# Kernel optimization log

Measured on AMD Instinct MI355X. Metric: run time of the kernel, lower is better.

## Reference

```python
import jax, jax.numpy as jnp
import numpy as np

N_NODES = 50000
N_EDGES = 800000
IN_FEATS = 96
HIDDEN = 48


def setup_inputs() -> dict:
    key = jax.random.key(0)
    ks = jax.random.split(key, 16)
    x = jax.random.normal(ks[0], (N_NODES, IN_FEATS), dtype=jnp.float32)
    edge_index = jax.random.randint(ks[1], (2, N_EDGES), 0, N_NODES, dtype=jnp.int32)

    def lin(k, fan_in, fan_out):
        s = 1.0 / np.sqrt(fan_in)
        return jax.random.uniform(k, (fan_in, fan_out), jnp.float32, -s, s)

    return {
        "x": x,
        "edge_index": edge_index,
        # SAGEConv layer 0: in -> hidden
        "w_self0": lin(ks[2], IN_FEATS, HIDDEN),
        "w_neigh0": lin(ks[3], IN_FEATS, HIDDEN),
        "b0": jnp.zeros((HIDDEN,), jnp.float32),
        # SAGEConv layer 1: hidden -> hidden
        "w_self1": lin(ks[4], HIDDEN, HIDDEN),
        "w_neigh1": lin(ks[5], HIDDEN, HIDDEN),
        "b1": jnp.zeros((HIDDEN,), jnp.float32),
        # SAGEConv layer 2: hidden -> hidden
        "w_self2": lin(ks[6], HIDDEN, HIDDEN),
        "w_neigh2": lin(ks[7], HIDDEN, HIDDEN),
        "b2": jnp.zeros((HIDDEN,), jnp.float32),
        # prediction head: hidden -> 1
        "w_pred": lin(ks[8], HIDDEN, 1),
        "b_pred": jnp.zeros((1,), jnp.float32),
    }


def _sage_mean(x, src, dst, deg_inv, w_self, w_neigh, b):
    # mean over in-neighbors: gather src features, segment-sum at dst, / in-degree
    agg = jax.ops.segment_sum(x[src], dst, num_segments=N_NODES) * deg_inv  # [N, F]
    return x @ w_self + agg @ w_neigh + b


def reference(x, edge_index, w_self0, w_neigh0, b0, w_self1, w_neigh1, b1,
              w_self2, w_neigh2, b2, w_pred, b_pred):
    src, dst = edge_index[0], edge_index[1]
    deg = jax.ops.segment_sum(jnp.ones((src.shape[0],), x.dtype), dst,
                              num_segments=N_NODES)
    deg_inv = (1.0 / jnp.maximum(deg, 1.0))[:, None]  # isolated nodes -> 0 agg

    h = jax.nn.relu(_sage_mean(x, src, dst, deg_inv, w_self0, w_neigh0, b0))
    h = jax.nn.relu(_sage_mean(h, src, dst, deg_inv, w_self1, w_neigh1, b1))
    h = jax.nn.relu(_sage_mean(h, src, dst, deg_inv, w_self2, w_neigh2, b2))
    return h @ w_pred + b_pred  # [N, 1]
```

## Files before the change

kernel.cpp:

```cpp
#include <hip/hip_runtime.h>
#include <hip/hip_fp16.h>


constexpr int HID = 48;
constexpr int MAXDEG = 64;
constexpr int GNB = 64;

__device__ __forceinline__ unsigned pack_h2(float a, float b) {
    __half2 h = __floats2half2_rn(a, b);
    return *reinterpret_cast<unsigned*>(&h);
}
__device__ __forceinline__ void acc_u2(float* g, uint2 u) {
    __half2 h0 = *reinterpret_cast<__half2*>(&u.x);
    __half2 h1 = *reinterpret_cast<__half2*>(&u.y);
    float2 f0 = __half22float2(h0), f1 = __half22float2(h1);
    g[0] += f0.x; g[1] += f0.y; g[2] += f1.x; g[3] += f1.y;
}
__device__ __forceinline__ void unpack_u2(float* v, uint2 u) {
    __half2 h0 = *reinterpret_cast<__half2*>(&u.x);
    __half2 h1 = *reinterpret_cast<__half2*>(&u.y);
    float2 f0 = __half22float2(h0), f1 = __half22float2(h1);
    v[0] = f0.x; v[1] = f0.y; v[2] = f1.x; v[3] = f1.y;
}
__device__ __forceinline__ void fma12_h(const uint2* __restrict__ wrow, float s,
                                        float* acc) {
    uint2 w0 = wrow[0], w1 = wrow[1], w2 = wrow[2];
    float v[12];
    unpack_u2(v + 0, w0); unpack_u2(v + 4, w1); unpack_u2(v + 8, w2);
#pragma unroll
    for (int j = 0; j < 12; ++j) acc[j] = fmaf(s, v[j], acc[j]);
}

__device__ __forceinline__ void gather_h8(const __half* __restrict__ p,
                                          const unsigned short* __restrict__ bkt,
                                          uint4 pv0, uint4 pv1, int deg, int e,
                                          int jb, int zrow, float* g) {
    float ga[12], gb[12];
#pragma unroll
    for (int j = 0; j < 12; ++j) { ga[j] = 0.0f; gb[j] = 0.0f; }
    const int sh = 16 * e;
    int idx[8];
    {
        unsigned w[8] = {pv0.x, pv0.y, pv0.z, pv0.w, pv1.x, pv1.y, pv1.z, pv1.w};
#pragma unroll
        for (int r = 0; r < 8; ++r) {
            int k = 2 * r + e;
            idx[r] = (k < deg) ? (int)((w[r] >> sh) & 0xffffu) : zrow;
        }
    }
    {
        const uint2* r0 = reinterpret_cast<const uint2*>(p + (size_t)idx[0] * HID + jb);
        const uint2* r1 = reinterpret_cast<const uint2*>(p + (size_t)idx[1] * HID + jb);
        const uint2* r2 = reinterpret_cast<const uint2*>(p + (size_t)idx[2] * HID + jb);
        const uint2* r3 = reinterpret_cast<const uint2*>(p + (size_t)idx[3] * HID + jb);
        uint2 a0 = r0[0], a1 = r0[1], a2 = r0[2];
        uint2 b0 = r1[0], b1 = r1[1], b2 = r1[2];
        uint2 c0 = r2[0], c1 = r2[1], c2 = r2[2];
        uint2 d0 = r3[0], d1 = r3[1], d2 = r3[2];
        acc_u2(ga + 0, a0); acc_u2(ga + 4, a1); acc_u2(ga + 8, a2);
        acc_u2(gb + 0, b0); acc_u2(gb + 4, b1); acc_u2(gb + 8, b2);
        acc_u2(ga + 0, c0); acc_u2(ga + 4, c1); acc_u2(ga + 8, c2);
        acc_u2(gb + 0, d0); acc_u2(gb + 4, d1); acc_u2(gb + 8, d2);
    }
    {
        const uint2* r0 = reinterpret_cast<const uint2*>(p + (size_t)idx[4] * HID + jb);
        const uint2* r1 = reinterpret_cast<const uint2*>(p + (size_t)idx[5] * HID + jb);
        const uint2* r2 = reinterpret_cast<const uint2*>(p + (size_t)idx[6] * HID + jb);
        const uint2* r3 = reinterpret_cast<const uint2*>(p + (size_t)idx[7] * HID + jb);
        uint2 a0 = r0[0], a1 = r0[1], a2 = r0[2];
        uint2 b0 = r1[0], b1 = r1[1], b2 = r1[2];
        uint2 c0 = r2[0], c1 = r2[1], c2 = r2[2];
        uint2 d0 = r3[0], d1 = r3[1], d2 = r3[2];
        acc_u2(ga + 0, a0); acc_u2(ga + 4, a1); acc_u2(ga + 8, a2);
        acc_u2(gb + 0, b0); acc_u2(gb + 4, b1); acc_u2(gb + 8, b2);
        acc_u2(ga + 0, c0); acc_u2(ga + 4, c1); acc_u2(ga + 8, c2);
        acc_u2(gb + 0, d0); acc_u2(gb + 4, d1); acc_u2(gb + 8, d2);
    }
    int i = 16 + e;
    for (; i + 6 < deg; i += 8) {
        int s0 = bkt[i], s1 = bkt[i + 2], s2 = bkt[i + 4], s3 = bkt[i + 6];
        const uint2* r0 = reinterpret_cast<const uint2*>(p + (size_t)s0 * HID + jb);
        const uint2* r1 = reinterpret_cast<const uint2*>(p + (size_t)s1 * HID + jb);
        const uint2* r2 = reinterpret_cast<const uint2*>(p + (size_t)s2 * HID + jb);
        const uint2* r3 = reinterpret_cast<const uint2*>(p + (size_t)s3 * HID + jb);
        uint2 a0 = r0[0], a1 = r0[1], a2 = r0[2];
        uint2 b0 = r1[0], b1 = r1[1], b2 = r1[2];
        uint2 c0 = r2[0], c1 = r2[1], c2 = r2[2];
        uint2 d0 = r3[0], d1 = r3[1], d2 = r3[2];
        acc_u2(ga + 0, a0); acc_u2(ga + 4, a1); acc_u2(ga + 8, a2);
        acc_u2(gb + 0, b0); acc_u2(gb + 4, b1); acc_u2(gb + 8, b2);
        acc_u2(ga + 0, c0); acc_u2(ga + 4, c1); acc_u2(ga + 8, c2);
        acc_u2(gb + 0, d0); acc_u2(gb + 4, d1); acc_u2(gb + 8, d2);
    }
    for (; i + 2 < deg; i += 4) {
        int s0 = bkt[i], s1 = bkt[i + 2];
        const uint2* r0 = reinterpret_cast<const uint2*>(p + (size_t)s0 * HID + jb);
        const uint2* r1 = reinterpret_cast<const uint2*>(p + (size_t)s1 * HID + jb);
        uint2 a0 = r0[0], a1 = r0[1], a2 = r0[2];
        uint2 b0 = r1[0], b1 = r1[1], b2 = r1[2];
        acc_u2(ga + 0, a0); acc_u2(ga + 4, a1); acc_u2(ga + 8, a2);
        acc_u2(gb + 0, b0); acc_u2(gb + 4, b1); acc_u2(gb + 8, b2);
    }
    if (i < deg) {
        const uint2* r0 = reinterpret_cast<const uint2*>(p + (size_t)bkt[i] * HID + jb);
        uint2 a0 = r0[0], a1 = r0[1], a2 = r0[2];
        acc_u2(ga + 0, a0); acc_u2(ga + 4, a1); acc_u2(ga + 8, a2);
    }
#pragma unroll
    for (int j = 0; j < 12; ++j) g[j] = ga[j] + gb[j];
#pragma unroll
    for (int j = 0; j < 12; ++j) g[j] += __shfl_xor(g[j], 4, 64);
}

__global__ __launch_bounds__(128) void fill_proj_k(
    const float* __restrict__ X, const float* __restrict__ Wn,
    const float* __restrict__ Ws, const float* __restrict__ bias,
    __half* __restrict__ p_out, float* __restrict__ s_out, int n_nodes,
    const int* __restrict__ src, const int* __restrict__ dst,
    int* __restrict__ cnt, unsigned short* __restrict__ buckets,
    int n_edges, int gemm_blocks, int cstride) {
    __shared__ float wlds[96 * HID];
    __shared__ float bias_lds[HID];
    const int t = threadIdx.x;

    if ((int)blockIdx.x >= gemm_blocks) {
        int base = (blockIdx.x - gemm_blocks) * 512 + t;
#pragma unroll
        for (int u = 0; u < 4; ++u) {
            int eidx = base + u * 128;
            if (eidx < n_edges) {
                int d = dst[eidx];
                int s = src[eidx];
                int pos = atomicAdd(&cnt[(size_t)d * cstride], 1);
                if (pos < MAXDEG) buckets[(size_t)d * MAXDEG + pos] = (unsigned short)s;
            }
        }
        return;
    }

    if (blockIdx.x == 0 && t < 24)
        reinterpret_cast<unsigned*>(p_out + (size_t)n_nodes * HID)[t] = 0u;

    const int q = t & 3;
    const int m = t >> 2;
    const int jb = q * 12;
    const int n0 = blockIdx.x * GNB + 2 * m;
    const int n1 = n0 + 1;
    const bool v0 = n0 < n_nodes, v1 = n1 < n_nodes;
    const int cn0 = v0 ? n0 : 0, cn1 = v1 ? n1 : 0;
    const float4* xr0 = reinterpret_cast<const float4*>(X + (size_t)cn0 * 96);
    const float4* xr1 = reinterpret_cast<const float4*>(X + (size_t)cn1 * 96);

    for (int i = t; i < 96 * HID; i += 128) wlds[i] = Wn[i];
    __syncthreads();
    {
        float pa[12], pb[12];
#pragma unroll
        for (int j = 0; j < 12; ++j) { pa[j] = 0.0f; pb[j] = 0.0f; }
#pragma unroll 4
        for (int k4 = 0; k4 < 24; ++k4) {
            float4 xa = xr0[k4];
            float4 xb = xr1[k4];
#pragma unroll
            for (int c = 0; c < 4; ++c) {
                float x0 = (c == 0) ? xa.x : (c == 1) ? xa.y : (c == 2) ? xa.z : xa.w;
                float x1 = (c == 0) ? xb.x : (c == 1) ? xb.y : (c == 2) ? xb.z : xb.w;
                const float4* wr =
                    reinterpret_cast<const float4*>(&wlds[(k4 * 4 + c) * HID + jb]);
#pragma unroll
                for (int j4 = 0; j4 < 3; ++j4) {
                    float4 wv = wr[j4];
                    pa[j4 * 4 + 0] = fmaf(x0, wv.x, pa[j4 * 4 + 0]);
                    pa[j4 * 4 + 1] = fmaf(x0, wv.y, pa[j4 * 4 + 1]);
                    pa[j4 * 4 + 2] = fmaf(x0, wv.z, pa[j4 * 4 + 2]);
                    pa[j4 * 4 + 3] = fmaf(x0, wv.w, pa[j4 * 4 + 3]);
                    pb[j4 * 4 + 0] = fmaf(x1, wv.x, pb[j4 * 4 + 0]);
                    pb[j4 * 4 + 1] = fmaf(x1, wv.y, pb[j4 * 4 + 1]);
                    pb[j4 * 4 + 2] = fmaf(x1, wv.z, pb[j4 * 4 + 2]);
                    pb[j4 * 4 + 3] = fmaf(x1, wv.w, pb[j4 * 4 + 3]);
                }
            }
        }
        if (v0) {
            uint2* po = reinterpret_cast<uint2*>(p_out + (size_t)n0 * HID + jb);
            po[0] = make_uint2(pack_h2(pa[0], pa[1]), pack_h2(pa[2], pa[3]));
            po[1] = make_uint2(pack_h2(pa[4], pa[5]), pack_h2(pa[6], pa[7]));
            po[2] = make_uint2(pack_h2(pa[8], pa[9]), pack_h2(pa[10], pa[11]));
        }
        if (v1) {
            uint2* po = reinterpret_cast<uint2*>(p_out + (size_t)n1 * HID + jb);
            po[0] = make_uint2(pack_h2(pb[0], pb[1]), pack_h2(pb[2], pb[3]));
            po[1] = make_uint2(pack_h2(pb[4], pb[5]), pack_h2(pb[6], pb[7]));
            po[2] = make_uint2(pack_h2(pb[8], pb[9]), pack_h2(pb[10], pb[11]));
        }
    }
    __syncthreads();

    for (int i = t; i < 96 * HID; i += 128) wlds[i] = Ws[i];
    if (t < HID) bias_lds[t] = bias[t];
    __syncthreads();
    {
        float sa[12], sb[12];
#pragma unroll
        for (int j = 0; j < 12; ++j) {
            float b = bias_lds[jb + j];
            sa[j] = b; sb[j] = b;
        }
#pragma unroll 4
        for (int k4 = 0; k4 < 24; ++k4) {
            float4 xa = xr0[k4];
            float4 xb = xr1[k4];
#pragma unroll
            for (int c = 0; c < 4; ++c) {
                float x0 = (c == 0) ? xa.x : (c == 1) ? xa.y : (c == 2) ? xa.z : xa.w;
                float x1 = (c == 0) ? xb.x : (c == 1) ? xb.y : (c == 2) ? xb.z : xb.w;
                const float4* wr =
                    reinterpret_cast<const float4*>(&wlds[(k4 * 4 + c) * HID + jb]);
#pragma unroll
                for (int j4 = 0; j4 < 3; ++j4) {
                    float4 wv = wr[j4];
                    sa[j4 * 4 + 0] = fmaf(x0, wv.x, sa[j4 * 4 + 0]);
                    sa[j4 * 4 + 1] = fmaf(x0, wv.y, sa[j4 * 4 + 1]);
                    sa[j4 * 4 + 2] = fmaf(x0, wv.z, sa[j4 * 4 + 2]);
                    sa[j4 * 4 + 3] = fmaf(x0, wv.w, sa[j4 * 4 + 3]);
                    sb[j4 * 4 + 0] = fmaf(x1, wv.x, sb[j4 * 4 + 0]);
                    sb[j4 * 4 + 1] = fmaf(x1, wv.y, sb[j4 * 4 + 1]);
                    sb[j4 * 4 + 2] = fmaf(x1, wv.z, sb[j4 * 4 + 2]);
                    sb[j4 * 4 + 3] = fmaf(x1, wv.w, sb[j4 * 4 + 3]);
                }
            }
        }
        float4* so0 = reinterpret_cast<float4*>(s_out + (size_t)cn0 * HID + jb);
        float4* so1 = reinterpret_cast<float4*>(s_out + (size_t)cn1 * HID + jb);
#pragma unroll
        for (int j4 = 0; j4 < 3; ++j4) {
            if (v0) so0[j4] = make_float4(sa[j4 * 4 + 0], sa[j4 * 4 + 1],
                                          sa[j4 * 4 + 2], sa[j4 * 4 + 3]);
            if (v1) so1[j4] = make_float4(sb[j4 * 4 + 0], sb[j4 * 4 + 1],
                                          sb[j4 * 4 + 2], sb[j4 * 4 + 3]);
        }
    }
}

__global__ __launch_bounds__(128, 6) void act_k(
    const __half* __restrict__ p_in, const float* __restrict__ s_in,
    const int* __restrict__ cnt, const unsigned short* __restrict__ buckets,
    __half* __restrict__ h_out, int n_nodes, int cstride) {
    const int t = threadIdx.x;
    if (blockIdx.x == 0 && t < 24)
        reinterpret_cast<unsigned*>(h_out + (size_t)n_nodes * HID)[t] = 0u;
    const int q = t & 3;
    const int e = (t >> 2) & 1;
    const int m = t >> 3;
    const int n = blockIdx.x * 16 + m;
    if (n >= n_nodes) return;
    const int jb = q * 12;

    const int deg_raw = cnt[(size_t)n * cstride];
    const unsigned short* bkt = buckets + (size_t)n * MAXDEG;
    const uint4 pv0 = reinterpret_cast<const uint4*>(bkt)[0];
    const uint4 pv1 = reinterpret_cast<const uint4*>(bkt)[1];
    float4 sv0, sv1, sv2;
    if (e == 0) {
        const float4* sr = reinterpret_cast<const float4*>(s_in + (size_t)n * HID + jb);
        sv0 = sr[0]; sv1 = sr[1]; sv2 = sr[2];
    }

    const int deg = min(deg_raw, MAXDEG);
    const float di = 1.0f / fmaxf((float)deg, 1.0f);
    float g[12];
    gather_h8(p_in, bkt, pv0, pv1, deg, e, jb, n_nodes, g);

    if (e == 0) {
        float h[12];
        h[0] = fmaxf(fmaf(di, g[0], sv0.x), 0.0f);
        h[1] = fmaxf(fmaf(di, g[1], sv0.y), 0.0f);
        h[2] = fmaxf(fmaf(di, g[2], sv0.z), 0.0f);
        h[3] = fmaxf(fmaf(di, g[3], sv0.w), 0.0f);
        h[4] = fmaxf(fmaf(di, g[4], sv1.x), 0.0f);
        h[5] = fmaxf(fmaf(di, g[5], sv1.y), 0.0f);
        h[6] = fmaxf(fmaf(di, g[6], sv1.z), 0.0f);
        h[7] = fmaxf(fmaf(di, g[7], sv1.w), 0.0f);
        h[8] = fmaxf(fmaf(di, g[8], sv2.x), 0.0f);
        h[9] = fmaxf(fmaf(di, g[9], sv2.y), 0.0f);
        h[10] = fmaxf(fmaf(di, g[10], sv2.z), 0.0f);
        h[11] = fmaxf(fmaf(di, g[11], sv2.w), 0.0f);
        uint2* ho = reinterpret_cast<uint2*>(h_out + (size_t)n * HID + jb);
        ho[0] = make_uint2(pack_h2(h[0], h[1]), pack_h2(h[2], h[3]));
        ho[1] = make_uint2(pack_h2(h[4], h[5]), pack_h2(h[6], h[7]));
        ho[2] = make_uint2(pack_h2(h[8], h[9]), pack_h2(h[10], h[11]));
    }
}

template <bool LAST>
__global__ __launch_bounds__(128, 6) void layer_k(
    const __half* __restrict__ h_in, const int* __restrict__ cnt,
    const unsigned short* __restrict__ buckets, const float* __restrict__ wn,
    const float* __restrict__ ws, const float* __restrict__ bn,
    const float* __restrict__ w_pred, const float* __restrict__ b_pred,
    __half* __restrict__ h_out, float* __restrict__ out, int n_nodes,
    int cstride) {
    __shared__ uint2 wn_s[HID * HID / 4];
    __shared__ uint2 ws_s[HID * HID / 4];
    __shared__ float bn_lds[HID];
    __shared__ float wp_lds[HID];

    const int t = threadIdx.x;
    const int q = t & 3;
    const int e = (t >> 2) & 1;
    const int m = t >> 3;
    const int n = blockIdx.x * 16 + m;
    const bool nv = n < n_nodes;
    const int cn = nv ? n : 0;
    const int jb = q * 12;

    if (!LAST && blockIdx.x == 0 && t < 24)
        reinterpret_cast<unsigned*>(h_out + (size_t)n_nodes * HID)[t] = 0u;

    const int deg_raw = cnt[(size_t)cn * cstride];
    const unsigned short* bkt = buckets + (size_t)cn * MAXDEG;
    const uint4 pv0 = reinterpret_cast<const uint4*>(bkt)[0];
    const uint4 pv1 = reinterpret_cast<const uint4*>(bkt)[1];
    const uint2* hr = reinterpret_cast<const uint2*>(h_in + (size_t)cn * HID + jb);
    uint2 ha = hr[0], hb = hr[1], hc = hr[2];

    for (int i4 = t; i4 < HID * HID / 4; i4 += 128) {
        float4 a = reinterpret_cast<const float4*>(wn)[i4];
        float4 b = reinterpret_cast<const float4*>(ws)[i4];
        wn_s[i4] = make_uint2(pack_h2(a.x, a.y), pack_h2(a.z, a.w));
        ws_s[i4] = make_uint2(pack_h2(b.x, b.y), pack_h2(b.z, b.w));
    }
    if (t < HID) bn_lds[t] = bn[t];
    if (LAST && t < HID) wp_lds[t] = w_pred[t];
    __syncthreads();

    if (!nv) return;

    const int deg = min(deg_raw, MAXDEG);
    const float di = 1.0f / fmaxf((float)deg, 1.0f);
    float g[12];
    gather_h8(h_in, bkt, pv0, pv1, deg, e, jb, n_nodes, g);
#pragma unroll
    for (int j = 0; j < 12; ++j) g[j] *= di;

    float hs_own[12];
    unpack_u2(hs_own + 0, ha); unpack_u2(hs_own + 4, hb); unpack_u2(hs_own + 8, hc);

    float acc[12];
#pragma unroll
    for (int j = 0; j < 12; ++j) acc[j] = (e == 0) ? bn_lds[jb + j] : 0.0f;

    const int kb = e * 24;
#pragma unroll
    for (int kk = 0; kk < 24; ++kk) {
        const int k = kb + kk;
        const int srcl = (t & ~3) | (k / 12);
        float gs = __shfl(g[kk % 12], srcl, 64);
        float hv = __shfl(hs_own[kk % 12], srcl, 64);
        fma12_h(&wn_s[(k * HID + jb) >> 2], gs, acc);
        fma12_h(&ws_s[(k * HID + jb) >> 2], hv, acc);
    }
#pragma unroll
    for (int j = 0; j < 12; ++j) acc[j] += __shfl_xor(acc[j], 4, 64);

    if (LAST) {
        float s = 0.0f;
#pragma unroll
        for (int j = 0; j < 12; ++j) s = fmaf(fmaxf(acc[j], 0.0f), wp_lds[jb + j], s);
        s += __shfl_xor(s, 1, 64);
        s += __shfl_xor(s, 2, 64);
        if ((t & 7) == 0) out[n] = s + b_pred[0];
        return;
    }

    if (e == 0) {
        float h[12];
#pragma unroll
        for (int j = 0; j < 12; ++j) h[j] = fmaxf(acc[j], 0.0f);
        uint2* ho = reinterpret_cast<uint2*>(h_out + (size_t)n * HID + jb);
        ho[0] = make_uint2(pack_h2(h[0], h[1]), pack_h2(h[2], h[3]));
        ho[1] = make_uint2(pack_h2(h[4], h[5]), pack_h2(h[6], h[7]));
        ho[2] = make_uint2(pack_h2(h[8], h[9]), pack_h2(h[10], h[11]));
    }
}

extern "C" void kernel_launch(void* const* d_in, const int* in_sizes, int n_in,
                              void* d_out, int out_size, void* d_ws, size_t ws_size,
                              hipStream_t stream) {
    const float* x        = (const float*)d_in[0];
    const int*   ei       = (const int*)d_in[1];
    const float* w_self0  = (const float*)d_in[2];
    const float* w_neigh0 = (const float*)d_in[3];
    const float* b0       = (const float*)d_in[4];
    const float* w_self1  = (const float*)d_in[5];
    const float* w_neigh1 = (const float*)d_in[6];
    const float* b1       = (const float*)d_in[7];
    const float* w_self2  = (const float*)d_in[8];
    const float* w_neigh2 = (const float*)d_in[9];
    const float* b2       = (const float*)d_in[10];
    const float* w_pred   = (const float*)d_in[11];
    const float* b_pred   = (const float*)d_in[12];

    const int n_nodes = in_sizes[0] / 96;
    const int n_edges = in_sizes[1] / 2;
    const int* src = ei;
    const int* dst = ei + n_edges;

    const size_t need_fixed = (size_t)n_nodes * MAXDEG * 2
                            + 3 * ((size_t)(n_nodes + 1) * HID * 2)
                            + (size_t)n_nodes * HID * 4;
    int cstride = (need_fixed + (size_t)n_nodes * 4 * 4 <= ws_size) ? 4 : 1;

    char* wsb = (char*)d_ws;
    int* cnt                = (int*)wsb;              wsb += (size_t)n_nodes * cstride * 4;
    unsigned short* buckets = (unsigned short*)wsb;   wsb += (size_t)n_nodes * MAXDEG * 2;
    __half* p0 = (__half*)wsb;                        wsb += (size_t)(n_nodes + 1) * HID * 2;
    __half* h1 = (__half*)wsb;                        wsb += (size_t)(n_nodes + 1) * HID * 2;
    __half* h2 = (__half*)wsb;                        wsb += (size_t)(n_nodes + 1) * HID * 2;
    float* s0 = (float*)wsb;                          wsb += (size_t)n_nodes * HID * 4;
    float* out = (float*)d_out;

    const int gnb = (n_nodes + GNB - 1) / GNB;
    const int fb = (n_edges + 511) / 512;
    const int lb = (n_nodes + 15) / 16;

    hipMemsetAsync(cnt, 0, (size_t)n_nodes * cstride * 4, stream);

    fill_proj_k<<<gnb + fb, 128, 0, stream>>>(x, w_neigh0, w_self0, b0, p0, s0,
                                              n_nodes, src, dst, cnt, buckets,
                                              n_edges, gnb, cstride);
    act_k<<<lb, 128, 0, stream>>>(p0, s0, cnt, buckets, h1, n_nodes, cstride);
    layer_k<false><<<lb, 128, 0, stream>>>(h1, cnt, buckets, w_neigh1, w_self1,
                                           b1, nullptr, nullptr, h2, nullptr,
                                           n_nodes, cstride);
    layer_k<true><<<lb, 128, 0, stream>>>(h2, cnt, buckets, w_neigh2, w_self2,
                                          b2, w_pred, b_pred, nullptr, out,
                                          n_nodes, cstride);
}
```

Measured before the change: 216.6 us.

## Gather neighbor rows with 16-byte loads, six lanes per node

Changes the gather lane mapping. Before, 8 lanes per node split the edges between two halves and each lane read 12 fp16 channels as three 8-byte loads. Now 6 of the 8 lanes each own 8 channels, read them with one 16-byte load per neighbor over all edges, and need no cross-lane reduction. The aim is fewer, wider memory instructions and no shuffle reduction. In exchange, 2 of every 8 lanes sit idle during the gather, each active lane walks twice as many edges, and the layer kernel's shuffle indexing is rewritten to match the new channel ownership.

Measured after the change: 280.3 us. 1.29x slower.

```diff
diff --git a/kernel.cpp b/kernel.cpp
--- a/kernel.cpp
+++ b/kernel.cpp
@@ -16,6 +16,10 @@
     float2 f0 = __half22float2(h0), f1 = __half22float2(h1);
     g[0] += f0.x; g[1] += f0.y; g[2] += f1.x; g[3] += f1.y;
 }
+__device__ __forceinline__ void acc_u4(float* g, uint4 u) {
+    acc_u2(g + 0, make_uint2(u.x, u.y));
+    acc_u2(g + 4, make_uint2(u.z, u.w));
+}
 __device__ __forceinline__ void unpack_u2(float* v, uint2 u) {
     __half2 h0 = *reinterpret_cast<__half2*>(&u.x);
     __half2 h1 = *reinterpret_cast<__half2*>(&u.y);
@@ -31,85 +35,51 @@
     for (int j = 0; j < 12; ++j) acc[j] = fmaf(s, v[j], acc[j]);
 }
 
-__device__ __forceinline__ void gather_h8(const __half* __restrict__ p,
-                                          const unsigned short* __restrict__ bkt,
-                                          uint4 pv0, uint4 pv1, int deg, int e,
-                                          int jb, int zrow, float* g) {
-    float ga[12], gb[12];
-#pragma unroll
-    for (int j = 0; j < 12; ++j) { ga[j] = 0.0f; gb[j] = 0.0f; }
-    const int sh = 16 * e;
-    int idx[8];
-    {
-        unsigned w[8] = {pv0.x, pv0.y, pv0.z, pv0.w, pv1.x, pv1.y, pv1.z, pv1.w};
-#pragma unroll
-        for (int r = 0; r < 8; ++r) {
-            int k = 2 * r + e;
-            idx[r] = (k < deg) ? (int)((w[r] >> sh) & 0xffffu) : zrow;
-        }
-    }
-    {
-        const uint2* r0 = reinterpret_cast<const uint2*>(p + (size_t)idx[0] * HID + jb);
-        const uint2* r1 = reinterpret_cast<const uint2*>(p + (size_t)idx[1] * HID + jb);
-        const uint2* r2 = reinterpret_cast<const uint2*>(p + (size_t)idx[2] * HID + jb);
-        const uint2* r3 = reinterpret_cast<const uint2*>(p + (size_t)idx[3] * HID + jb);
-        uint2 a0 = r0[0], a1 = r0[1], a2 = r0[2];
-        uint2 b0 = r1[0], b1 = r1[1], b2 = r1[2];
-        uint2 c0 = r2[0], c1 = r2[1], c2 = r2[2];
-        uint2 d0 = r3[0], d1 = r3[1], d2 = r3[2];
-        acc_u2(ga + 0, a0); acc_u2(ga + 4, a1); acc_u2(ga + 8, a2);
-        acc_u2(gb + 0, b0); acc_u2(gb + 4, b1); acc_u2(gb + 8, b2);
-        acc_u2(ga + 0, c0); acc_u2(ga + 4, c1); acc_u2(ga + 8, c2);
-        acc_u2(gb + 0, d0); acc_u2(gb + 4, d1); acc_u2(gb + 8, d2);
-    }
-    {
-        const uint2* r0 = reinterpret_cast<const uint2*>(p + (size_t)idx[4] * HID + jb);
-        const uint2* r1 = reinterpret_cast<const uint2*>(p + (size_t)idx[5] * HID + jb);
-        const uint2* r2 = reinterpret_cast<const uint2*>(p + (size_t)idx[6] * HID + jb);
-        const uint2* r3 = reinterpret_cast<const uint2*>(p + (size_t)idx[7] * HID + jb);
-        uint2 a0 = r0[0], a1 = r0[1], a2 = r0[2];
-        uint2 b0 = r1[0], b1 = r1[1], b2 = r1[2];
-        uint2 c0 = r2[0], c1 = r2[1], c2 = r2[2];
-        uint2 d0 = r3[0], d1 = r3[1], d2 = r3[2];
-        acc_u2(ga + 0, a0); acc_u2(ga + 4, a1); acc_u2(ga + 8, a2);
-        acc_u2(gb + 0, b0); acc_u2(gb + 4, b1); acc_u2(gb + 8, b2);
-        acc_u2(ga + 0, c0); acc_u2(ga + 4, c1); acc_u2(ga + 8, c2);
-        acc_u2(gb + 0, d0); acc_u2(gb + 4, d1); acc_u2(gb + 8, d2);
-    }
-    int i = 16 + e;
-    for (; i + 6 < deg; i += 8) {
-        int s0 = bkt[i], s1 = bkt[i + 2], s2 = bkt[i + 4], s3 = bkt[i + 6];
-        const uint2* r0 = reinterpret_cast<const uint2*>(p + (size_t)s0 * HID + jb);
-        const uint2* r1 = reinterpret_cast<const uint2*>(p + (size_t)s1 * HID + jb);
-        const uint2* r2 = reinterpret_cast<const uint2*>(p + (size_t)s2 * HID + jb);
-        const uint2* r3 = reinterpret_cast<const uint2*>(p + (size_t)s3 * HID + jb);
-        uint2 a0 = r0[0], a1 = r0[1], a2 = r0[2];
-        uint2 b0 = r1[0], b1 = r1[1], b2 = r1[2];
-        uint2 c0 = r2[0], c1 = r2[1], c2 = r2[2];
-        uint2 d0 = r3[0], d1 = r3[1], d2 = r3[2];
-        acc_u2(ga + 0, a0); acc_u2(ga + 4, a1); acc_u2(ga + 8, a2);
-        acc_u2(gb + 0, b0); acc_u2(gb + 4, b1); acc_u2(gb + 8, b2);
-        acc_u2(ga + 0, c0); acc_u2(ga + 4, c1); acc_u2(ga + 8, c2);
-        acc_u2(gb + 0, d0); acc_u2(gb + 4, d1); acc_u2(gb + 8, d2);
-    }
-    for (; i + 2 < deg; i += 4) {
-        int s0 = bkt[i], s1 = bkt[i + 2];
-        const uint2* r0 = reinterpret_cast<const uint2*>(p + (size_t)s0 * HID + jb);
-        const uint2* r1 = reinterpret_cast<const uint2*>(p + (size_t)s1 * HID + jb);
-        uint2 a0 = r0[0], a1 = r0[1], a2 = r0[2];
-        uint2 b0 = r1[0], b1 = r1[1], b2 = r1[2];
-        acc_u2(ga + 0, a0); acc_u2(ga + 4, a1); acc_u2(ga + 8, a2);
-        acc_u2(gb + 0, b0); acc_u2(gb + 4, b1); acc_u2(gb + 8, b2);
-    }
-    if (i < deg) {
-        const uint2* r0 = reinterpret_cast<const uint2*>(p + (size_t)bkt[i] * HID + jb);
-        uint2 a0 = r0[0], a1 = r0[1], a2 = r0[2];
-        acc_u2(ga + 0, a0); acc_u2(ga + 4, a1); acc_u2(ga + 8, a2);
-    }
-#pragma unroll
-    for (int j = 0; j < 12; ++j) g[j] = ga[j] + gb[j];
-#pragma unroll
-    for (int j = 0; j < 12; ++j) g[j] += __shfl_xor(g[j], 4, 64);
+__device__ __forceinline__ void gather8(const __half* __restrict__ p,
+                                        const unsigned short* __restrict__ bkt,
+                                        const uint4 (&pw)[2], int deg,
+                                        int coff, int zrow, float* g) {
+    float ga[8], gb[8];
+#pragma unroll
+    for (int c = 0; c < 8; ++c) { ga[c] = 0.0f; gb[c] = 0.0f; }
+#pragma unroll
+    for (int b = 0; b < 2; ++b) {
+        const int k0 = 8 * b;
+        const unsigned w0 = pw[b].x, w1 = pw[b].y, w2 = pw[b].z, w3 = pw[b].w;
+        int i0 = (k0 + 0 < deg) ? (int)(w0 & 0xffffu) : zrow;
+        int i1 = (k0 + 1 < deg) ? (int)(w0 >> 16) : zrow;
+        int i2 = (k0 + 2 < deg) ? (int)(w1 & 0xffffu) : zrow;
+        int i3 = (k0 + 3 < deg) ? (int)(w1 >> 16) : zrow;
+        int i4 = (k0 + 4 < deg) ? (int)(w2 & 0xffffu) : zrow;
+        int i5 = (k0 + 5 < deg) ? (int)(w2 >> 16) : zrow;
+        int i6 = (k0 + 6 < deg) ? (int)(w3 & 0xffffu) : zrow;
+        int i7 = (k0 + 7 < deg) ? (int)(w3 >> 16) : zrow;
+        uint4 a0 = *reinterpret_cast<const uint4*>(p + (size_t)i0 * HID + coff);
+        uint4 a1 = *reinterpret_cast<const uint4*>(p + (size_t)i1 * HID + coff);
+        uint4 a2 = *reinterpret_cast<const uint4*>(p + (size_t)i2 * HID + coff);
+        uint4 a3 = *reinterpret_cast<const uint4*>(p + (size_t)i3 * HID + coff);
+        uint4 a4 = *reinterpret_cast<const uint4*>(p + (size_t)i4 * HID + coff);
+        uint4 a5 = *reinterpret_cast<const uint4*>(p + (size_t)i5 * HID + coff);
+        uint4 a6 = *reinterpret_cast<const uint4*>(p + (size_t)i6 * HID + coff);
+        uint4 a7 = *reinterpret_cast<const uint4*>(p + (size_t)i7 * HID + coff);
+        acc_u4(ga, a0); acc_u4(gb, a1); acc_u4(ga, a2); acc_u4(gb, a3);
+        acc_u4(ga, a4); acc_u4(gb, a5); acc_u4(ga, a6); acc_u4(gb, a7);
+    }
+    int i = 16;
+    for (; i + 3 < deg; i += 4) {
+        int s0 = bkt[i], s1 = bkt[i + 1], s2 = bkt[i + 2], s3 = bkt[i + 3];
+        uint4 a0 = *reinterpret_cast<const uint4*>(p + (size_t)s0 * HID + coff);
+        uint4 a1 = *reinterpret_cast<const uint4*>(p + (size_t)s1 * HID + coff);
+        uint4 a2 = *reinterpret_cast<const uint4*>(p + (size_t)s2 * HID + coff);
+        uint4 a3 = *reinterpret_cast<const uint4*>(p + (size_t)s3 * HID + coff);
+        acc_u4(ga, a0); acc_u4(gb, a1); acc_u4(ga, a2); acc_u4(gb, a3);
+    }
+    for (; i < deg; ++i) {
+        uint4 a0 = *reinterpret_cast<const uint4*>(p + (size_t)bkt[i] * HID + coff);
+        acc_u4(ga, a0);
+    }
+#pragma unroll
+    for (int c = 0; c < 8; ++c) g[c] = ga[c] + gb[c];
 }
 
 __global__ __launch_bounds__(128) void fill_proj_k(
@@ -249,47 +219,42 @@
     const int t = threadIdx.x;
     if (blockIdx.x == 0 && t < 24)
         reinterpret_cast<unsigned*>(h_out + (size_t)n_nodes * HID)[t] = 0u;
-    const int q = t & 3;
-    const int e = (t >> 2) & 1;
+
+    const int cid = t & 7;
     const int m = t >> 3;
     const int n = blockIdx.x * 16 + m;
     if (n >= n_nodes) return;
-    const int jb = q * 12;
+    const bool active = cid < 6;
+    const int cb = active ? 8 * cid : 0;
 
     const int deg_raw = cnt[(size_t)n * cstride];
     const unsigned short* bkt = buckets + (size_t)n * MAXDEG;
-    const uint4 pv0 = reinterpret_cast<const uint4*>(bkt)[0];
-    const uint4 pv1 = reinterpret_cast<const uint4*>(bkt)[1];
-    float4 sv0, sv1, sv2;
-    if (e == 0) {
-        const float4* sr = reinterpret_cast<const float4*>(s_in + (size_t)n * HID + jb);
-        sv0 = sr[0]; sv1 = sr[1]; sv2 = sr[2];
-    }
+    uint4 pw[2];
+#pragma unroll
+    for (int b = 0; b < 2; ++b) pw[b] = reinterpret_cast<const uint4*>(bkt)[b];
+
+    if (!active) return;
 
     const int deg = min(deg_raw, MAXDEG);
     const float di = 1.0f / fmaxf((float)deg, 1.0f);
-    float g[12];
-    gather_h8(p_in, bkt, pv0, pv1, deg, e, jb, n_nodes, g);
-
-    if (e == 0) {
-        float h[12];
-        h[0] = fmaxf(fmaf(di, g[0], sv0.x), 0.0f);
-        h[1] = fmaxf(fmaf(di, g[1], sv0.y), 0.0f);
-        h[2] = fmaxf(fmaf(di, g[2], sv0.z), 0.0f);
-        h[3] = fmaxf(fmaf(di, g[3], sv0.w), 0.0f);
-        h[4] = fmaxf(fmaf(di, g[4], sv1.x), 0.0f);
-        h[5] = fmaxf(fmaf(di, g[5], sv1.y), 0.0f);
-        h[6] = fmaxf(fmaf(di, g[6], sv1.z), 0.0f);
-        h[7] = fmaxf(fmaf(di, g[7], sv1.w), 0.0f);
-        h[8] = fmaxf(fmaf(di, g[8], sv2.x), 0.0f);
-        h[9] = fmaxf(fmaf(di, g[9], sv2.y), 0.0f);
-        h[10] = fmaxf(fmaf(di, g[10], sv2.z), 0.0f);
-        h[11] = fmaxf(fmaf(di, g[11], sv2.w), 0.0f);
-        uint2* ho = reinterpret_cast<uint2*>(h_out + (size_t)n * HID + jb);
-        ho[0] = make_uint2(pack_h2(h[0], h[1]), pack_h2(h[2], h[3]));
-        ho[1] = make_uint2(pack_h2(h[4], h[5]), pack_h2(h[6], h[7]));
-        ho[2] = make_uint2(pack_h2(h[8], h[9]), pack_h2(h[10], h[11]));
-    }
+
+    float g[8];
+    gather8(p_in, bkt, pw, deg, cb, n_nodes, g);
+
+    const float4* sr = reinterpret_cast<const float4*>(s_in + (size_t)n * HID + cb);
+    float4 s0v = sr[0], s1v = sr[1];
+    float h[8];
+    h[0] = fmaxf(fmaf(di, g[0], s0v.x), 0.0f);
+    h[1] = fmaxf(fmaf(di, g[1], s0v.y), 0.0f);
+    h[2] = fmaxf(fmaf(di, g[2], s0v.z), 0.0f);
+    h[3] = fmaxf(fmaf(di, g[3], s0v.w), 0.0f);
+    h[4] = fmaxf(fmaf(di, g[4], s1v.x), 0.0f);
+    h[5] = fmaxf(fmaf(di, g[5], s1v.y), 0.0f);
+    h[6] = fmaxf(fmaf(di, g[6], s1v.z), 0.0f);
+    h[7] = fmaxf(fmaf(di, g[7], s1v.w), 0.0f);
+    uint4 o = make_uint4(pack_h2(h[0], h[1]), pack_h2(h[2], h[3]),
+                         pack_h2(h[4], h[5]), pack_h2(h[6], h[7]));
+    *reinterpret_cast<uint4*>(h_out + (size_t)n * HID + cb) = o;
 }
 
 template <bool LAST>
@@ -306,12 +271,15 @@
     __shared__ float wp_lds[HID];
 
     const int t = threadIdx.x;
+    const int cid = t & 7;
     const int q = t & 3;
     const int e = (t >> 2) & 1;
     const int m = t >> 3;
     const int n = blockIdx.x * 16 + m;
     const bool nv = n < n_nodes;
     const int cn = nv ? n : 0;
+    const bool active = cid < 6;
+    const int cb = active ? 8 * cid : 0;
     const int jb = q * 12;
 
     if (!LAST && blockIdx.x == 0 && t < 24)
@@ -319,10 +287,10 @@
 
     const int deg_raw = cnt[(size_t)cn * cstride];
     const unsigned short* bkt = buckets + (size_t)cn * MAXDEG;
-    const uint4 pv0 = reinterpret_cast<const uint4*>(bkt)[0];
-    const uint4 pv1 = reinterpret_cast<const uint4*>(bkt)[1];
-    const uint2* hr = reinterpret_cast<const uint2*>(h_in + (size_t)cn * HID + jb);
-    uint2 ha = hr[0], hb = hr[1], hc = hr[2];
+    uint4 pw[2];
+#pragma unroll
+    for (int b = 0; b < 2; ++b) pw[b] = reinterpret_cast<const uint4*>(bkt)[b];
+    uint4 hv4 = *reinterpret_cast<const uint4*>(h_in + (size_t)cn * HID + cb);
 
     for (int i4 = t; i4 < HID * HID / 4; i4 += 128) {
         float4 a = reinterpret_cast<const float4*>(wn)[i4];
@@ -338,25 +306,32 @@
 
     const int deg = min(deg_raw, MAXDEG);
     const float di = 1.0f / fmaxf((float)deg, 1.0f);
-    float g[12];
-    gather_h8(h_in, bkt, pv0, pv1, deg, e, jb, n_nodes, g);
-#pragma unroll
-    for (int j = 0; j < 12; ++j) g[j] *= di;
-
-    float hs_own[12];
-    unpack_u2(hs_own + 0, ha); unpack_u2(hs_own + 4, hb); unpack_u2(hs_own + 8, hc);
+    float g[8];
+    if (active) {
+        gather8(h_in, bkt, pw, deg, cb, n_nodes, g);
+#pragma unroll
+        for (int c = 0; c < 8; ++c) g[c] *= di;
+    } else {
+#pragma unroll
+        for (int c = 0; c < 8; ++c) g[c] = 0.0f;
+    }
+
+    float hs[8];
+    unpack_u2(hs + 0, make_uint2(hv4.x, hv4.y));
+    unpack_u2(hs + 4, make_uint2(hv4.z, hv4.w));
 
     float acc[12];
 #pragma unroll
     for (int j = 0; j < 12; ++j) acc[j] = (e == 0) ? bn_lds[jb + j] : 0.0f;
 
-    const int kb = e * 24;
+    const int e24 = e * 24;
+    const int e3 = e * 3;
 #pragma unroll
     for (int kk = 0; kk < 24; ++kk) {
-        const int k = kb + kk;
-        const int srcl = (t & ~3) | (k / 12);
-        float gs = __shfl(g[kk % 12], srcl, 64);
-        float hv = __shfl(hs_own[kk % 12], srcl, 64);
+        const int k = e24 + kk;
+        const int srcl = (t & ~7) | (e3 + (kk >> 3));
+        float gs = __shfl(g[kk & 7], srcl, 64);
+        float hv = __shfl(hs[kk & 7], srcl, 64);
         fma12_h(&wn_s[(k * HID + jb) >> 2], gs, acc);
         fma12_h(&ws_s[(k * HID + jb) >> 2], hv, acc);
     }
```
